# Optimization experiments

Hardware: AMD Instinct MI355X
Metric: run time of the kernel (lower is better)

Reference implementation:

```python
import jax, jax.numpy as jnp
import numpy as np

DIM, HID, NC = 512, 102, 64
B, NS, ND, M = 256, 196, 196, 40
EPS_LN = 1e-5


def setup_inputs() -> dict:
    key = jax.random.key(0)
    ks = jax.random.split(key, 8)
    s = lambda d: 1.0 / np.sqrt(d)
    return {
        "tokens_sparse": jax.random.normal(ks[0], (B, NS, DIM), jnp.float32),
        "tokens_dense": jax.random.normal(ks[1], (B, ND, DIM), jnp.float32),
        "words": jax.random.normal(ks[2], (B, M, DIM), jnp.float32),
        "ln_g_s": jnp.ones((DIM,), jnp.float32),
        "ln_b_s": jnp.zeros((DIM,), jnp.float32),
        "w1_s": jax.random.normal(ks[3], (DIM, HID), jnp.float32) * s(DIM),
        "b1_s": jnp.zeros((HID,), jnp.float32),
        "w2_s": jax.random.normal(ks[4], (HID, NC), jnp.float32) * s(HID),
        "b2_s": jnp.zeros((NC,), jnp.float32),
        "ln_g_d": jnp.ones((DIM,), jnp.float32),
        "ln_b_d": jnp.zeros((DIM,), jnp.float32),
        "w1_d": jax.random.normal(ks[5], (DIM, HID), jnp.float32) * s(DIM),
        "b1_d": jnp.zeros((HID,), jnp.float32),
        "w2_d": jax.random.normal(ks[6], (HID, NC), jnp.float32) * s(HID),
        "b2_d": jnp.zeros((NC,), jnp.float32),
        "scale": jnp.ones((1, 1, 1), jnp.float32),
    }


def _layernorm(x, g, b):
    mu = x.mean(-1, keepdims=True)
    var = ((x - mu) ** 2).mean(-1, keepdims=True)
    return (x - mu) * jax.lax.rsqrt(var + EPS_LN) * g + b


def _aggregate(x, ln_g, ln_b, w1, b1, w2, b2, scale):
    # weight = MLP(LN(x)) -> (B, N, NC); transpose -> (B, NC, N); softmax over N; bmm
    h = jax.nn.gelu(_layernorm(x, ln_g, ln_b) @ w1 + b1, approximate=False)
    w = jnp.swapaxes(h @ w2 + b2, 1, 2) * scale            # (B, NC, N)
    w = jax.nn.softmax(w, axis=2)
    return jnp.einsum("bkn,bnc->bkc", w, x)                 # (B, NC, C)


def _l2norm(x):
    return x / jnp.maximum(jnp.linalg.norm(x, axis=-1, keepdims=True), 1e-8)


def reference(tokens_sparse, tokens_dense, words,
              ln_g_s, ln_b_s, w1_s, b1_s, w2_s, b2_s,
              ln_g_d, ln_b_d, w1_d, b1_d, w2_d, b2_d, scale):
    # DualTokenAggregation: paper Eq.(4)
    agg = _aggregate(tokens_sparse, ln_g_s, ln_b_s, w1_s, b1_s, w2_s, b2_s, scale)
    agg = agg + _aggregate(tokens_dense, ln_g_d, ln_b_d, w1_d, b1_d, w2_d, b2_d, scale)
    v = _l2norm(agg)                                        # (B, NC, C)
    t = _l2norm(words)                                      # (B, M, C)
    # HRPA (scan=True, bidirectional, no mask): bmm + leaky_relu + max/mean pooling
    sim = jnp.einsum("bmc,bkc->bmk", t, v)                  # (B, M, NC)
    sim = jnp.where(sim >= 0, sim, 0.1 * sim)               # leaky_relu(0.1)
    row_mean = sim.max(axis=2).mean(axis=1, keepdims=True)  # word->patch
    col_mean = sim.max(axis=1).mean(axis=1, keepdims=True)  # patch->word
    return row_mean + col_mean                              # (B, 1)
```

## Files before the change

### kernel.cpp

```cpp
#include <hip/hip_runtime.h>
#include <math.h>

#define Bb 256
#define Nn 196
#define Dd 512
#define Hh 102
#define Kk 64
#define Mm 40

#define LOGITS_BYTES 25690112
#define W1H_OFF  ((size_t)25690112)
#define W1L_OFF  (W1H_OFF + 262144)
#define GWB1_OFF (W1L_OFF + 262144)
#define W2TH_OFF (GWB1_OFF + 2048)
#define W2TL_OFF (W2TH_OFF + 32768)
#define AGG_OFF  (W2TL_OFF + 32768)

using short8 = __attribute__((ext_vector_type(8))) short;
using f32x4  = __attribute__((ext_vector_type(4))) float;

__device__ __forceinline__ void barrier_lgkm_only() {
  asm volatile("s_waitcnt lgkmcnt(0)" ::: "memory");
  __builtin_amdgcn_s_barrier();
  asm volatile("" ::: "memory");
}

__device__ __forceinline__ float dot4(const float4 a, const float4 b) {
  return a.x*b.x + a.y*b.y + a.z*b.z + a.w*b.w;
}
__device__ __forceinline__ float4 ld4s(const float* p) { return *(const float4*)p; }
__device__ __forceinline__ float gelu1(float z) {
  return 0.5f * z * (1.f + erff(z * 0.70710678118f));
}
__device__ __forceinline__ unsigned short bf16hi(float v) {
  return (unsigned short)(__float_as_uint(v) >> 16);
}
__device__ __forceinline__ float hipart(float v) {
  return __uint_as_float(__float_as_uint(v) & 0xffff0000u);
}
__device__ __forceinline__ void split8(const float4 va, const float4 vb,
                                       short8& hh, short8& ll) {
  hh[0] = (short)bf16hi(va.x); ll[0] = (short)bf16hi(va.x - hipart(va.x));
  hh[1] = (short)bf16hi(va.y); ll[1] = (short)bf16hi(va.y - hipart(va.y));
  hh[2] = (short)bf16hi(va.z); ll[2] = (short)bf16hi(va.z - hipart(va.z));
  hh[3] = (short)bf16hi(va.w); ll[3] = (short)bf16hi(va.w - hipart(va.w));
  hh[4] = (short)bf16hi(vb.x); ll[4] = (short)bf16hi(vb.x - hipart(vb.x));
  hh[5] = (short)bf16hi(vb.y); ll[5] = (short)bf16hi(vb.y - hipart(vb.y));
  hh[6] = (short)bf16hi(vb.z); ll[6] = (short)bf16hi(vb.z - hipart(vb.z));
  hh[7] = (short)bf16hi(vb.w); ll[7] = (short)bf16hi(vb.w - hipart(vb.w));
}
__device__ __forceinline__ float wave_reduce_sum(float v) {
#pragma unroll
  for (int o = 1; o < 64; o <<= 1) v += __shfl_xor(v, o, 64);
  return v;
}
__device__ __forceinline__ float wave_reduce_max(float v) {
#pragma unroll
  for (int o = 1; o < 64; o <<= 1) v = fmaxf(v, __shfl_xor(v, o, 64));
  return v;
}

__global__ __launch_bounds__(512) void k0_wprep(
    const float* __restrict__ g_s, const float* __restrict__ b_s,
    const float* __restrict__ w1_s, const float* __restrict__ b1_s,
    const float* __restrict__ w2_s,
    const float* __restrict__ g_d, const float* __restrict__ b_d,
    const float* __restrict__ w1_d, const float* __restrict__ b1_d,
    const float* __restrict__ w2_d,
    unsigned short* __restrict__ w1h, unsigned short* __restrict__ w1l,
    float* __restrict__ gwb1,
    unsigned short* __restrict__ w2th, unsigned short* __restrict__ w2tl)
{
  const int p = blockIdx.x, slice = blockIdx.y;
  const float* g  = p ? g_d  : g_s;
  const float* bb = p ? b_d  : b_s;
  const float* w1 = p ? w1_d : w1_s;
  const float* b1 = p ? b1_d : b1_s;
  const float* w2 = p ? w2_d : w2_s;
  const int tid = threadIdx.x;

  if (slice < 8) {
    for (int idx = slice * 8192 + tid; idx < slice * 8192 + 8192; idx += 512) {
      const int j = idx & 127, c = idx >> 7;
      const float v = (j < Hh) ? w1[(size_t)c * Hh + j] * g[c] : 0.f;
      w1h[((size_t)(p * 128 + j)) * 512 + c] = bf16hi(v);
      w1l[((size_t)(p * 128 + j)) * 512 + c] = bf16hi(v - hipart(v));
    }
  } else {
    for (int idx = tid; idx < 8192; idx += 512) {
      const int k = idx >> 7, j = idx & 127;
      const float v = (j < Hh) ? w2[(size_t)j * Kk + k] : 0.f;
      w2th[(size_t)(p * 64 + k) * 128 + j] = bf16hi(v);
      w2tl[(size_t)(p * 64 + k) * 128 + j] = bf16hi(v - hipart(v));
    }
  }

  if (slice == 0) {
    __shared__ float red[4][128][2];
    const int j = tid & 127, part = tid >> 7;
    float sg = 0.f, sb = 0.f;
    if (j < Hh) {
      for (int c = part * 128; c < part * 128 + 128; ++c) {
        const float w = w1[(size_t)c * Hh + j];
        sg += g[c] * w;
        sb += bb[c] * w;
      }
    }
    red[part][j][0] = sg;
    red[part][j][1] = sb;
    __syncthreads();
    if (part == 0) {
      const float G  = red[0][j][0] + red[1][j][0] + red[2][j][0] + red[3][j][0];
      const float Bv = red[0][j][1] + red[1][j][1] + red[2][j][1] + red[3][j][1];
      gwb1[(p * 128 + j) * 2]     = G;
      gwb1[(p * 128 + j) * 2 + 1] = (j < Hh) ? (Bv + b1[j]) : 0.f;
    }
  }
}

__global__ __launch_bounds__(512) void k1_logits(
    const float* __restrict__ x_s, const float* __restrict__ x_d,
    const unsigned short* __restrict__ w1h, const unsigned short* __restrict__ w1l,
    const float* __restrict__ gwb1,
    const unsigned short* __restrict__ w2th, const unsigned short* __restrict__ w2tl,
    const float* __restrict__ b2_s, const float* __restrict__ b2_d,
    float* __restrict__ logits)
{
  __shared__ __align__(16) char smem1[40320];
  unsigned short* xbuf = (unsigned short*)smem1;
  unsigned short* hs_h = (unsigned short*)smem1;
  unsigned short* hs_l = (unsigned short*)(smem1 + 16128);
  float* part = (float*)(smem1 + 35840);
  float* st   = (float*)(smem1 + 39424);

  const int tid = threadIdx.x;
  const int ntile = blockIdx.x, p = blockIdx.y, b = blockIdx.z;
  const int nbase = ntile * 112;
  const float* x  = p ? x_d : x_s;
  const float* b2 = p ? b2_d : b2_s;

  const int lane = tid & 63, wv = tid >> 6;
  const int lr = lane & 15, lg = lane >> 4;
  const int jb = wv * 16;
  const unsigned short* wph = w1h + ((size_t)(p * 128 + jb + lr)) * 512 + lg * 8;
  const unsigned short* wpl = w1l + ((size_t)(p * 128 + jb + lr)) * 512 + lg * 8;

  const int t = tid >> 2, q = tid & 3;
  const bool stg = (tid < 448);
  const int n = nbase + t;
  const bool valid = stg && (n < Nn);
  const float* xrow = x + ((size_t)(b * Nn + (valid ? n : 0))) * Dd + q * 8;

  float psum = 0.f, psq = 0.f;
  f32x4 acc0 = {0,0,0,0}, acc1 = acc0, acc2 = acc0, acc3 = acc0;
  f32x4 acc4 = acc0, acc5 = acc0, acc6 = acc0;

  short8 bh_c = *(const short8*)(wph);
  short8 bl_c = *(const short8*)(wpl);

  {
    float4 va = {0,0,0,0}, vb = va;
    if (valid) { va = ld4s(xrow); vb = ld4s(xrow + 4); }
    if (stg) {
      psum += va.x + va.y + va.z + va.w + vb.x + vb.y + vb.z + vb.w;
      psq  += dot4(va, va) + dot4(vb, vb);
      short8 hh, ll;
      split8(va, vb, hh, ll);
      *(short8*)(xbuf + t * 40 + q * 8) = hh;
      *(short8*)(xbuf + 4480 + t * 40 + q * 8) = ll;
    }
  }
  barrier_lgkm_only();

#pragma unroll 1
  for (int ch = 0; ch < 16; ++ch) {
    const int buf = ch & 1;
    const unsigned short* xh = xbuf + buf * 8960;
    const unsigned short* xl = xh + 4480;

    short8 bh_n = bh_c, bl_n = bl_c;
    float4 va = {0,0,0,0}, vb = va;
    if (ch < 15) {
      const int co = (ch + 1) * 32;
      bh_n = *(const short8*)(wph + co);
      bl_n = *(const short8*)(wpl + co);
      if (valid) { va = ld4s(xrow + co); vb = ld4s(xrow + co + 4); }
    }

#define MSTEP(A, M) { \
    const short8 ah = *(const short8*)(xh + ((M) * 16 + lr) * 40 + lg * 8); \
    const short8 al = *(const short8*)(xl + ((M) * 16 + lr) * 40 + lg * 8); \
    (A) = __builtin_amdgcn_mfma_f32_16x16x32_bf16(ah, bh_c, (A), 0, 0, 0); \
    (A) = __builtin_amdgcn_mfma_f32_16x16x32_bf16(ah, bl_c, (A), 0, 0, 0); \
    (A) = __builtin_amdgcn_mfma_f32_16x16x32_bf16(al, bh_c, (A), 0, 0, 0); }
    MSTEP(acc0, 0) MSTEP(acc1, 1) MSTEP(acc2, 2) MSTEP(acc3, 3)
    MSTEP(acc4, 4) MSTEP(acc5, 5) MSTEP(acc6, 6)
#undef MSTEP

    if (ch < 15 && stg) {
      psum += va.x + va.y + va.z + va.w + vb.x + vb.y + vb.z + vb.w;
      psq  += dot4(va, va) + dot4(vb, vb);
      short8 hh, ll;
      split8(va, vb, hh, ll);
      unsigned short* xw = xbuf + (buf ^ 1) * 8960;
      *(short8*)(xw + t * 40 + q * 8) = hh;
      *(short8*)(xw + 4480 + t * 40 + q * 8) = ll;
    }
    bh_c = bh_n; bl_c = bl_n;
    barrier_lgkm_only();
  }

  if (stg) {
    part[t * 8 + q * 2]     = psum;
    part[t * 8 + q * 2 + 1] = psq;
  }
  __syncthreads();
  if (tid < 112) {
    const float s  = part[tid * 8] + part[tid * 8 + 2] + part[tid * 8 + 4] + part[tid * 8 + 6];
    const float ss = part[tid * 8 + 1] + part[tid * 8 + 3] + part[tid * 8 + 5] + part[tid * 8 + 7];
    const float mu  = s * (1.f / 512.f);
    const float var = fmaxf(ss * (1.f / 512.f) - mu * mu, 0.f);
    st[2 * tid]     = mu;
    st[2 * tid + 1] = rsqrtf(var + 1e-5f);
  }
  __syncthreads();

  const int colw = jb + lr;
  const float Gw = gwb1[(p * 128 + colw) * 2];
  const float B1 = gwb1[(p * 128 + colw) * 2 + 1];
  const int hwv  = wv >> 2;
  const int jloc = colw & 63;

#define HW1(A, M) { \
    _Pragma("unroll") \
    for (int rr = 0; rr < 4; ++rr) { \
      const int row = (M) * 16 + lg * 4 + rr; \
      const float mu = st[2 * row], rs = st[2 * row + 1]; \
      const float hv = gelu1(rs * (A)[rr] - mu * rs * Gw + B1); \
      hs_h[row * 72 + jloc] = bf16hi(hv); \
      hs_l[row * 72 + jloc] = bf16hi(hv - hipart(hv)); \
    } }
#define HWALL { HW1(acc0,0) HW1(acc1,1) HW1(acc2,2) HW1(acc3,3) \
                HW1(acc4,4) HW1(acc5,5) HW1(acc6,6) }

  f32x4 C0 = {0,0,0,0}, C1 = C0, C2 = C0, C3 = C0;
  const unsigned short* w2hb = w2th + (size_t)p * 8192 + lr * 128 + lg * 8;
  const unsigned short* w2lb = w2tl + (size_t)p * 8192 + lr * 128 + lg * 8;
  const int arow = (wv * 16 + lr) * 72 + lg * 8;

#define P2STEP(JG) { \
    const short8 Ah = *(const short8*)(hs_h + arow + ((JG) & 63)); \
    const short8 Al = *(const short8*)(hs_l + arow + ((JG) & 63)); \
    const short8 Bh0 = *(const short8*)(w2hb + (JG)); \
    const short8 Bl0 = *(const short8*)(w2lb + (JG)); \
    const short8 Bh1 = *(const short8*)(w2hb + 16 * 128 + (JG)); \
    const short8 Bl1 = *(const short8*)(w2lb + 16 * 128 + (JG)); \
    const short8 Bh2 = *(const short8*)(w2hb + 32 * 128 + (JG)); \
    const short8 Bl2 = *(const short8*)(w2lb + 32 * 128 + (JG)); \
    const short8 Bh3 = *(const short8*)(w2hb + 48 * 128 + (JG)); \
    const short8 Bl3 = *(const short8*)(w2lb + 48 * 128 + (JG)); \
    C0 = __builtin_amdgcn_mfma_f32_16x16x32_bf16(Ah, Bh0, C0, 0, 0, 0); \
    C0 = __builtin_amdgcn_mfma_f32_16x16x32_bf16(Ah, Bl0, C0, 0, 0, 0); \
    C0 = __builtin_amdgcn_mfma_f32_16x16x32_bf16(Al, Bh0, C0, 0, 0, 0); \
    C1 = __builtin_amdgcn_mfma_f32_16x16x32_bf16(Ah, Bh1, C1, 0, 0, 0); \
    C1 = __builtin_amdgcn_mfma_f32_16x16x32_bf16(Ah, Bl1, C1, 0, 0, 0); \
    C1 = __builtin_amdgcn_mfma_f32_16x16x32_bf16(Al, Bh1, C1, 0, 0, 0); \
    C2 = __builtin_amdgcn_mfma_f32_16x16x32_bf16(Ah, Bh2, C2, 0, 0, 0); \
    C2 = __builtin_amdgcn_mfma_f32_16x16x32_bf16(Ah, Bl2, C2, 0, 0, 0); \
    C2 = __builtin_amdgcn_mfma_f32_16x16x32_bf16(Al, Bh2, C2, 0, 0, 0); \
    C3 = __builtin_amdgcn_mfma_f32_16x16x32_bf16(Ah, Bh3, C3, 0, 0, 0); \
    C3 = __builtin_amdgcn_mfma_f32_16x16x32_bf16(Ah, Bl3, C3, 0, 0, 0); \
    C3 = __builtin_amdgcn_mfma_f32_16x16x32_bf16(Al, Bh3, C3, 0, 0, 0); }

  if (hwv == 0) { HWALL }
  __syncthreads();
  if (wv < 7) { P2STEP(0) P2STEP(32) }
  __syncthreads();
  if (hwv == 1) { HWALL }
  __syncthreads();
  if (wv < 7) { P2STEP(64) P2STEP(96) }
#undef P2STEP
#undef HWALL
#undef HW1

  if (wv < 7) {
    const float bb0 = b2[lr], bb1 = b2[16 + lr];
    const float bb2 = b2[32 + lr], bb3 = b2[48 + lr];
#pragma unroll
    for (int rr = 0; rr < 4; ++rr) {
      const int tok = wv * 16 + lg * 4 + rr;
      const int nn = nbase + tok;
      if (nn < Nn) {
        float* lgp = logits + ((size_t)(b * 2 + p) * Nn + nn) * Kk;
        lgp[lr]      = C0[rr] + bb0;
        lgp[16 + lr] = C1[rr] + bb1;
        lgp[32 + lr] = C2[rr] + bb2;
        lgp[48 + lr] = C3[rr] + bb3;
      }
    }
  }
}

__global__ __launch_bounds__(512) void k2_softmax_agg(
    const float* __restrict__ x_s, const float* __restrict__ x_d,
    const float* __restrict__ logits, const float* __restrict__ scale,
    float* __restrict__ aggP)
{
  __shared__ __align__(16) unsigned char smem2[63616];
  unsigned short* wth = (unsigned short*)smem2;
  unsigned short* wtl = (unsigned short*)(smem2 + 14848);
  unsigned short* xh2 = (unsigned short*)(smem2 + 29696);
  unsigned short* xl2 = (unsigned short*)(smem2 + 44544);
  float* rskA = (float*)(smem2 + 59392);
  float* redf = (float*)(smem2 + 59520);
  float* mxkA = (float*)(smem2 + 59520 + 2304);
  f32x4* redacc = (f32x4*)(smem2 + 59520);

  const int tid = threadIdx.x;
  const int p = blockIdx.x, b = blockIdx.y, ks = blockIdx.z;
  const float sc = scale[0];
  const float* xb = (p ? x_d : x_s) + (size_t)b * Nn * Dd;

  const int kloc = tid & 31, sprt = tid >> 5;
  const float* lgp = logits + ((size_t)(b * 2 + p) * Nn) * Kk + ks * 32 + kloc;
  float mx = -1e30f;
  for (int nn = sprt; nn < Nn; nn += 16) mx = fmaxf(mx, lgp[nn * 64] * sc);
  redf[sprt * 36 + kloc] = mx;
  __syncthreads();
  if (tid < 32) {
    float m = redf[tid];
#pragma unroll
    for (int gg = 1; gg < 16; ++gg) m = fmaxf(m, redf[gg * 36 + tid]);
    mxkA[tid] = m;
  }
  __syncthreads();
  const float mk = mxkA[kloc];
  float ssum = 0.f;
  for (int nn = sprt; nn < Nn; nn += 16) {
    const float e = expf(lgp[nn * 64] * sc - mk);
    wth[kloc * 232 + nn] = bf16hi(e);
    wtl[kloc * 232 + nn] = bf16hi(e - hipart(e));
    ssum += e;
  }
  for (int nn = Nn + sprt; nn < 224; nn += 16) {
    wth[kloc * 232 + nn] = 0;
    wtl[kloc * 232 + nn] = 0;
  }
  redf[sprt * 36 + kloc] = ssum;
  __syncthreads();
  if (tid < 32) {
    float s = 0.f;
#pragma unroll
    for (int gg = 0; gg < 16; ++gg) s += redf[gg * 36 + tid];
    rskA[tid] = 1.f / s;
  }

  const int lane = tid & 63, w = tid >> 6;
  const int lr = lane & 15, lg = lane >> 4;
  const int mt = w & 1, nt = (w >> 1) & 1, kh = w >> 2;
  const unsigned short* wthp = wth + (mt * 16 + lr) * 232 + lg * 8;
  const unsigned short* wtlp = wtl + (mt * 16 + lr) * 232 + lg * 8;
  const unsigned short* xh2p = xh2 + (nt * 16 + lr) * 232 + lg * 8;
  const unsigned short* xl2p = xl2 + (nt * 16 + lr) * 232 + lg * 8;
  const int s0 = kh ? 4 : 0, s1 = kh ? 7 : 4;
  const size_t agbase = ((size_t)((p * Bb + b) * Kk + ks * 32)) * Dd;

#pragma unroll 1
  for (int chn = 0; chn < 16; ++chn) {
    const int c0 = chn * 32;
    float vals[14];
#pragma unroll
    for (int ps = 0; ps < 14; ++ps) {
      const int idx = ps * 512 + tid;
      const int nn = idx >> 5;
      vals[ps] = (nn < Nn) ? xb[(size_t)nn * Dd + c0 + (idx & 31)] : 0.f;
    }
#pragma unroll
    for (int ps = 0; ps < 14; ++ps) {
      const int idx = ps * 512 + tid;
      const int nn = idx >> 5, cl = idx & 31;
      const float v = vals[ps];
      xh2[cl * 232 + nn] = bf16hi(v);
      xl2[cl * 232 + nn] = bf16hi(v - hipart(v));
    }
    barrier_lgkm_only();

    f32x4 acc = {0.f, 0.f, 0.f, 0.f};
#pragma unroll
    for (int s = s0; s < s1; ++s) {
      const int n0 = s * 32;
      const short8 ah = *(const short8*)(wthp + n0);
      const short8 al = *(const short8*)(wtlp + n0);
      const short8 bh = *(const short8*)(xh2p + n0);
      const short8 bl = *(const short8*)(xl2p + n0);
      acc = __builtin_amdgcn_mfma_f32_16x16x32_bf16(ah, bh, acc, 0, 0, 0);
      acc = __builtin_amdgcn_mfma_f32_16x16x32_bf16(ah, bl, acc, 0, 0, 0);
      acc = __builtin_amdgcn_mfma_f32_16x16x32_bf16(al, bh, acc, 0, 0, 0);
    }
    if (kh) redacc[(w - 4) * 64 + lane] = acc;
    barrier_lgkm_only();
    if (!kh) {
      const f32x4 o = redacc[w * 64 + lane];
#pragma unroll
      for (int rr = 0; rr < 4; ++rr) {
        const int kl2 = mt * 16 + lg * 4 + rr;
        aggP[agbase + (size_t)kl2 * Dd + c0 + nt * 16 + lr] =
            (acc[rr] + o[rr]) * rskA[kl2];
      }
    }
  }
}

__global__ __launch_bounds__(512) void k4_final(
    const float* __restrict__ words, const float* __restrict__ aggP,
    float* __restrict__ outp)
{
  __shared__ __align__(16) unsigned char vls[64 * 512];
  __shared__ float rowm[40];
  __shared__ float colp[8][72];
  const int tid = threadIdx.x, b = blockIdx.x;
  const int w = tid >> 6, lane = tid & 63;
  const float* a0  = aggP + (size_t)b * (Kk * Dd);
  const float* a1  = aggP + ((size_t)(Bb + b)) * (Kk * Dd);
  const float* wrd = words + (size_t)b * Mm * Dd;
  const int m0 = w * 5;

  float rnt0, rnt1, rnt2, rnt3, rnt4;
#define TNORM(R, I) { \
    const float* tr = wrd + (size_t)(m0 + (I)) * Dd + lane * 8; \
    float4 ta = ld4s(tr), tb = ld4s(tr + 4); \
    float ss = wave_reduce_sum(dot4(ta, ta) + dot4(tb, tb)); \
    R = 1.f / fmaxf(sqrtf(ss), 1e-8f); }
  TNORM(rnt0, 0) TNORM(rnt1, 1) TNORM(rnt2, 2) TNORM(rnt3, 3) TNORM(rnt4, 4)
#undef TNORM

  float acc0 = 0.f, acc1 = 0.f, acc2 = 0.f, acc3 = 0.f, acc4 = 0.f, vsq = 0.f;

#pragma unroll 1
  for (int chn = 0; chn < 4; ++chn) {
    const int c0 = chn * 128;
    __syncthreads();
#pragma unroll
    for (int s = 0; s < 4; ++s) {
      const int idx = tid + s * 512;
      const int k = idx >> 5, gc = idx & 31;
      const float4 u = ld4s(a0 + (size_t)k * Dd + c0 + gc * 4);
      const float4 v = ld4s(a1 + (size_t)k * Dd + c0 + gc * 4);
      float4 sv = {u.x + v.x, u.y + v.y, u.z + v.z, u.w + v.w};
      *(float4*)(vls + k * 512 + ((gc ^ (k & 31)) << 4)) = sv;
    }
    __syncthreads();
#pragma unroll 2
    for (int cc = 0; cc < 32; ++cc) {
      const float4 vv = *(const float4*)(vls + lane * 512 + ((cc ^ (lane & 31)) << 4));
      const float* tp = wrd + c0 + cc * 4;
      const float4 t0 = ld4s(tp + (size_t)(m0    ) * Dd);
      const float4 t1 = ld4s(tp + (size_t)(m0 + 1) * Dd);
      const float4 t2 = ld4s(tp + (size_t)(m0 + 2) * Dd);
      const float4 t3 = ld4s(tp + (size_t)(m0 + 3) * Dd);
      const float4 t4 = ld4s(tp + (size_t)(m0 + 4) * Dd);
      acc0 += dot4(t0, vv); acc1 += dot4(t1, vv); acc2 += dot4(t2, vv);
      acc3 += dot4(t3, vv); acc4 += dot4(t4, vv);
      vsq  += dot4(vv, vv);
    }
  }

  const float rnv = 1.f / fmaxf(sqrtf(vsq), 1e-8f);
  float cmax = -1e30f;
#define DOM(ACC, RNT, I) { \
    float s = (ACC) * (RNT) * rnv; \
    s = (s >= 0.f) ? s : 0.1f * s; \
    cmax = fmaxf(cmax, s); \
    float rm = wave_reduce_max(s); \
    if (lane == 0) rowm[m0 + (I)] = rm; }
  DOM(acc0, rnt0, 0) DOM(acc1, rnt1, 1) DOM(acc2, rnt2, 2)
  DOM(acc3, rnt3, 3) DOM(acc4, rnt4, 4)
#undef DOM
  colp[w][lane] = cmax;
  __syncthreads();
  if (w == 0) {
    float cm = colp[0][lane];
#pragma unroll
    for (int ww = 1; ww < 8; ++ww) cm = fmaxf(cm, colp[ww][lane]);
    const float csum = wave_reduce_sum(cm);
    const float rv = (lane < 40) ? rowm[lane] : 0.f;
    const float rsum = wave_reduce_sum(rv);
    if (lane == 0) outp[b] = rsum * (1.f / 40.f) + csum * (1.f / 64.f);
  }
}

extern "C" void kernel_launch(void* const* d_in, const int* in_sizes, int n_in,
                              void* d_out, int out_size, void* d_ws, size_t ws_size,
                              hipStream_t stream)
{
  const float* x_s   = (const float*)d_in[0];
  const float* x_d   = (const float*)d_in[1];
  const float* words = (const float*)d_in[2];
  const float* g_s   = (const float*)d_in[3];
  const float* b_s   = (const float*)d_in[4];
  const float* w1_s  = (const float*)d_in[5];
  const float* b1_s  = (const float*)d_in[6];
  const float* w2_s  = (const float*)d_in[7];
  const float* b2_s  = (const float*)d_in[8];
  const float* g_d   = (const float*)d_in[9];
  const float* b_d   = (const float*)d_in[10];
  const float* w1_d  = (const float*)d_in[11];
  const float* b1_d  = (const float*)d_in[12];
  const float* w2_d  = (const float*)d_in[13];
  const float* b2_d  = (const float*)d_in[14];
  const float* scale = (const float*)d_in[15];
  (void)in_sizes; (void)n_in; (void)out_size; (void)ws_size;

  char* ws = (char*)d_ws;
  float* logits        = (float*)ws;
  unsigned short* w1h  = (unsigned short*)(ws + W1H_OFF);
  unsigned short* w1l  = (unsigned short*)(ws + W1L_OFF);
  float* gwb1          = (float*)(ws + GWB1_OFF);
  unsigned short* w2th = (unsigned short*)(ws + W2TH_OFF);
  unsigned short* w2tl = (unsigned short*)(ws + W2TL_OFF);
  float* aggP          = (float*)(ws + AGG_OFF);

  hipLaunchKernelGGL(k0_wprep, dim3(2, 9), dim3(512), 0, stream,
                     g_s, b_s, w1_s, b1_s, w2_s, g_d, b_d, w1_d, b1_d, w2_d,
                     w1h, w1l, gwb1, w2th, w2tl);
  hipLaunchKernelGGL(k1_logits, dim3(2, 2, 256), dim3(512), 0, stream,
                     x_s, x_d, w1h, w1l, gwb1, w2th, w2tl,
                     b2_s, b2_d, logits);
  hipLaunchKernelGGL(k2_softmax_agg, dim3(2, Bb, 2), dim3(512), 0, stream,
                     x_s, x_d, logits, scale, aggP);
  hipLaunchKernelGGL(k4_final, dim3(256), dim3(512), 0, stream,
                     words, aggP, (float*)d_out);
}
```

Baseline: 323.1 us.

## Merge k-split in softmax-aggregate kernel, keep weights in registers, double-buffer x staging

The softmax-aggregate kernel now covers all 64 clusters in one block instead of splitting them across two blocks along a z-dimension. Each token tensor is therefore read from global memory once per (branch, batch) rather than twice. The softmax weight fragments are loaded once into registers, which removes the cross-wave accumulator reduction. The x chunks are double-buffered in LDS with an XOR swizzle so the next chunk can be staged while MFMAs run on the current one. The trade-off is half as many blocks and more LDS and register use per block, which may lower occupancy.

```diff
diff --git a/kernel.cpp b/kernel.cpp
--- a/kernel.cpp
+++ b/kernel.cpp
@@ -306,109 +306,128 @@
     const float* __restrict__ logits, const float* __restrict__ scale,
     float* __restrict__ aggP)
 {
-  __shared__ __align__(16) unsigned char smem2[63616];
-  unsigned short* wth = (unsigned short*)smem2;
-  unsigned short* wtl = (unsigned short*)(smem2 + 14848);
-  unsigned short* xh2 = (unsigned short*)(smem2 + 29696);
-  unsigned short* xl2 = (unsigned short*)(smem2 + 44544);
-  float* rskA = (float*)(smem2 + 59392);
-  float* redf = (float*)(smem2 + 59520);
-  float* mxkA = (float*)(smem2 + 59520 + 2304);
-  f32x4* redacc = (f32x4*)(smem2 + 59520);
+  __shared__ __align__(16) unsigned char smem2[68224];
+  unsigned short* eh = (unsigned short*)smem2;
+  unsigned short* el = (unsigned short*)(smem2 + 32768);
+  float* rsk  = (float*)(smem2 + 65536);
+  float* redf = (float*)(smem2 + 65792);
+  float* mxk  = (float*)(smem2 + 67968);
 
   const int tid = threadIdx.x;
-  const int p = blockIdx.x, b = blockIdx.y, ks = blockIdx.z;
+  const int p = blockIdx.x, b = blockIdx.y;
   const float sc = scale[0];
   const float* xb = (p ? x_d : x_s) + (size_t)b * Nn * Dd;
 
-  const int kloc = tid & 31, sprt = tid >> 5;
-  const float* lgp = logits + ((size_t)(b * 2 + p) * Nn) * Kk + ks * 32 + kloc;
+  const int kloc = tid & 63, sprt = tid >> 6;
+  const float* lgp = logits + ((size_t)(b * 2 + p) * Nn) * Kk + kloc;
+  const int eswz = (kloc & 7) << 3;
   float mx = -1e30f;
-  for (int nn = sprt; nn < Nn; nn += 16) mx = fmaxf(mx, lgp[nn * 64] * sc);
-  redf[sprt * 36 + kloc] = mx;
-  __syncthreads();
-  if (tid < 32) {
+  for (int nn = sprt; nn < Nn; nn += 8) mx = fmaxf(mx, lgp[nn * 64] * sc);
+  redf[sprt * 68 + kloc] = mx;
+  __syncthreads();
+  if (tid < 64) {
     float m = redf[tid];
 #pragma unroll
-    for (int gg = 1; gg < 16; ++gg) m = fmaxf(m, redf[gg * 36 + tid]);
-    mxkA[tid] = m;
-  }
-  __syncthreads();
-  const float mk = mxkA[kloc];
+    for (int gg = 1; gg < 8; ++gg) m = fmaxf(m, redf[gg * 68 + tid]);
+    mxk[tid] = m;
+  }
+  __syncthreads();
+  const float mk = mxk[kloc];
   float ssum = 0.f;
-  for (int nn = sprt; nn < Nn; nn += 16) {
+  for (int nn = sprt; nn < Nn; nn += 8) {
     const float e = expf(lgp[nn * 64] * sc - mk);
-    wth[kloc * 232 + nn] = bf16hi(e);
-    wtl[kloc * 232 + nn] = bf16hi(e - hipart(e));
+    const int ph = kloc * 256 + (nn ^ eswz);
+    eh[ph] = bf16hi(e);
+    el[ph] = bf16hi(e - hipart(e));
     ssum += e;
   }
-  for (int nn = Nn + sprt; nn < 224; nn += 16) {
-    wth[kloc * 232 + nn] = 0;
-    wtl[kloc * 232 + nn] = 0;
-  }
-  redf[sprt * 36 + kloc] = ssum;
-  __syncthreads();
-  if (tid < 32) {
+  for (int nn = Nn + sprt; nn < 224; nn += 8) {
+    const int ph = kloc * 256 + (nn ^ eswz);
+    eh[ph] = 0; el[ph] = 0;
+  }
+  redf[sprt * 68 + kloc] = ssum;
+  __syncthreads();
+  if (tid < 64) {
     float s = 0.f;
 #pragma unroll
-    for (int gg = 0; gg < 16; ++gg) s += redf[gg * 36 + tid];
-    rskA[tid] = 1.f / s;
-  }
-
-  const int lane = tid & 63, w = tid >> 6;
+    for (int gg = 0; gg < 8; ++gg) s += redf[gg * 68 + tid];
+    rsk[tid] = 1.f / s;
+  }
+  __syncthreads();
+
+  const int lane = tid & 63, wv = tid >> 6;
   const int lr = lane & 15, lg = lane >> 4;
-  const int mt = w & 1, nt = (w >> 1) & 1, kh = w >> 2;
-  const unsigned short* wthp = wth + (mt * 16 + lr) * 232 + lg * 8;
-  const unsigned short* wtlp = wtl + (mt * 16 + lr) * 232 + lg * 8;
-  const unsigned short* xh2p = xh2 + (nt * 16 + lr) * 232 + lg * 8;
-  const unsigned short* xl2p = xl2 + (nt * 16 + lr) * 232 + lg * 8;
-  const int s0 = kh ? 4 : 0, s1 = kh ? 7 : 4;
-  const size_t agbase = ((size_t)((p * Bb + b) * Kk + ks * 32)) * Dd;
+  const int kt = wv & 3, ct = wv >> 2;
+  const int arow = kt * 16 + lr;
+  const int aswz = (arow & 7) << 3;
+  const unsigned short* ebh = eh + arow * 256;
+  const unsigned short* ebl = el + arow * 256;
+  short8 Ah0, Ah1, Ah2, Ah3, Ah4, Ah5, Ah6;
+  short8 Al0, Al1, Al2, Al3, Al4, Al5, Al6;
+#define LDA(I) { const int off = ((I) * 32 + lg * 8) ^ aswz; \
+  Ah##I = *(const short8*)(ebh + off); \
+  Al##I = *(const short8*)(ebl + off); }
+  LDA(0) LDA(1) LDA(2) LDA(3) LDA(4) LDA(5) LDA(6)
+#undef LDA
+  const int kbase = kt * 16 + lg * 4;
+  const float r0 = rsk[kbase], r1 = rsk[kbase + 1];
+  const float r2 = rsk[kbase + 2], r3 = rsk[kbase + 3];
+  barrier_lgkm_only();
+
+  const int brow = ct * 16 + lr;
+  const int bswz = (brow & 7) << 3;
+  const size_t agk = (size_t)((p * Bb + b) * Kk + kbase) * Dd;
+
+#define K2STAGE(CHN, BUF) { \
+    const int c0s = (CHN) * 32; \
+    unsigned short* th = (unsigned short*)(smem2 + (BUF) * 32768); \
+    unsigned short* tl = (unsigned short*)(smem2 + (BUF) * 32768 + 16384); \
+    float vals[14]; \
+    _Pragma("unroll") \
+    for (int it = 0; it < 14; ++it) { \
+      const int idx = it * 512 + tid; \
+      const int nn = idx >> 5; \
+      vals[it] = (nn < Nn) ? xb[(size_t)nn * Dd + c0s + (idx & 31)] : 0.f; \
+    } \
+    _Pragma("unroll") \
+    for (int it = 0; it < 14; ++it) { \
+      const int idx = it * 512 + tid; \
+      const int nn = idx >> 5, cl = idx & 31; \
+      const float v = vals[it]; \
+      const int ph = cl * 256 + (nn ^ ((cl & 7) << 3)); \
+      th[ph] = bf16hi(v); \
+      tl[ph] = bf16hi(v - hipart(v)); \
+    } }
+
+  K2STAGE(0, 0)
+  barrier_lgkm_only();
 
 #pragma unroll 1
   for (int chn = 0; chn < 16; ++chn) {
-    const int c0 = chn * 32;
-    float vals[14];
-#pragma unroll
-    for (int ps = 0; ps < 14; ++ps) {
-      const int idx = ps * 512 + tid;
-      const int nn = idx >> 5;
-      vals[ps] = (nn < Nn) ? xb[(size_t)nn * Dd + c0 + (idx & 31)] : 0.f;
-    }
-#pragma unroll
-    for (int ps = 0; ps < 14; ++ps) {
-      const int idx = ps * 512 + tid;
-      const int nn = idx >> 5, cl = idx & 31;
-      const float v = vals[ps];
-      xh2[cl * 232 + nn] = bf16hi(v);
-      xl2[cl * 232 + nn] = bf16hi(v - hipart(v));
-    }
+    const int buf = chn & 1;
+    if (chn < 15) { K2STAGE(chn + 1, buf ^ 1) }
+
+    const unsigned short* bhb = (const unsigned short*)(smem2 + buf * 32768) + brow * 256;
+    const unsigned short* blb = (const unsigned short*)(smem2 + buf * 32768 + 16384) + brow * 256;
+    f32x4 acc = {0.f, 0.f, 0.f, 0.f};
+#define K2KS(I) { \
+    const int off = ((I) * 32 + lg * 8) ^ bswz; \
+    const short8 Bh = *(const short8*)(bhb + off); \
+    const short8 Bl = *(const short8*)(blb + off); \
+    acc = __builtin_amdgcn_mfma_f32_16x16x32_bf16(Ah##I, Bh, acc, 0, 0, 0); \
+    acc = __builtin_amdgcn_mfma_f32_16x16x32_bf16(Ah##I, Bl, acc, 0, 0, 0); \
+    acc = __builtin_amdgcn_mfma_f32_16x16x32_bf16(Al##I, Bh, acc, 0, 0, 0); }
+    K2KS(0) K2KS(1) K2KS(2) K2KS(3) K2KS(4) K2KS(5) K2KS(6)
+#undef K2KS
+
+    const int cc = chn * 32 + ct * 16 + lr;
+    aggP[agk              + cc] = acc[0] * r0;
+    aggP[agk +     (size_t)Dd + cc] = acc[1] * r1;
+    aggP[agk + 2 * (size_t)Dd + cc] = acc[2] * r2;
+    aggP[agk + 3 * (size_t)Dd + cc] = acc[3] * r3;
     barrier_lgkm_only();
-
-    f32x4 acc = {0.f, 0.f, 0.f, 0.f};
-#pragma unroll
-    for (int s = s0; s < s1; ++s) {
-      const int n0 = s * 32;
-      const short8 ah = *(const short8*)(wthp + n0);
-      const short8 al = *(const short8*)(wtlp + n0);
-      const short8 bh = *(const short8*)(xh2p + n0);
-      const short8 bl = *(const short8*)(xl2p + n0);
-      acc = __builtin_amdgcn_mfma_f32_16x16x32_bf16(ah, bh, acc, 0, 0, 0);
-      acc = __builtin_amdgcn_mfma_f32_16x16x32_bf16(ah, bl, acc, 0, 0, 0);
-      acc = __builtin_amdgcn_mfma_f32_16x16x32_bf16(al, bh, acc, 0, 0, 0);
-    }
-    if (kh) redacc[(w - 4) * 64 + lane] = acc;
-    barrier_lgkm_only();
-    if (!kh) {
-      const f32x4 o = redacc[w * 64 + lane];
-#pragma unroll
-      for (int rr = 0; rr < 4; ++rr) {
-        const int kl2 = mt * 16 + lg * 4 + rr;
-        aggP[agbase + (size_t)kl2 * Dd + c0 + nt * 16 + lr] =
-            (acc[rr] + o[rr]) * rskA[kl2];
-      }
-    }
-  }
+  }
+#undef K2STAGE
 }
 
 __global__ __launch_bounds__(512) void k4_final(
@@ -526,7 +545,7 @@
   hipLaunchKernelGGL(k1_logits, dim3(2, 2, 256), dim3(512), 0, stream,
                      x_s, x_d, w1h, w1l, gwb1, w2th, w2tl,
                      b2_s, b2_d, logits);
-  hipLaunchKernelGGL(k2_softmax_agg, dim3(2, Bb, 2), dim3(512), 0, stream,
+  hipLaunchKernelGGL(k2_softmax_agg, dim3(2, Bb), dim3(512), 0, stream,
                      x_s, x_d, logits, scale, aggP);
   hipLaunchKernelGGL(k4_final, dim3(256), dim3(512), 0, stream,
                      words, aggP, (float*)d_out);
```

New measurement: 303.6 us. 1.06x faster.
